# Optimization experiments

Hardware: AMD Instinct MI355X
Metric: run time of the kernel (lower is better)

Reference implementation:

```python
import jax, jax.numpy as jnp
import numpy as np

IN_F = 4096
OUT_F = 4096
BLOCK = 8
N_CENTROIDS = 2048
N_BLOCKS = IN_F // BLOCK  # 512
N_TOKENS = 1024


def setup_inputs() -> dict:
    key = jax.random.key(0)
    k1, k2, k3, k4 = jax.random.split(key, 4)
    x = jax.random.normal(k1, (N_TOKENS, IN_F), dtype=jnp.float32)
    centroids = jax.random.normal(k2, (N_CENTROIDS, BLOCK), dtype=jnp.float32)
    # assignments: block-major layout, length n_blocks * out_features
    assignments = jax.random.randint(k3, (N_BLOCKS * OUT_F,), 0, N_CENTROIDS, dtype=jnp.int32)
    bias = jax.random.normal(k4, (OUT_F,), dtype=jnp.float32) * 0.01
    # counts = bincount(assignments), used only in backward (grad averaging)
    counts = jax.ops.segment_sum(
        jnp.ones_like(assignments, dtype=jnp.float32), assignments,
        num_segments=N_CENTROIDS)
    return {"x": x, "centroids": centroids, "bias": bias,
            "assignments": assignments, "counts": counts}


def reference(x, centroids, bias, assignments, counts):
    # weight = centroids[assignments].reshape(n_blocks, out_f, block)
    #                        .permute(1,0,2).reshape(out_f, in_f)
    w = centroids[assignments]  # [n_blocks*out_f, block]
    w = w.reshape(N_BLOCKS, OUT_F, BLOCK).transpose(1, 0, 2).reshape(OUT_F, IN_F)
    # F.linear(x, weight, bias) = x @ w.T + bias
    return x @ w.T + bias
```

## Files before the change

### kernel.cpp

```cpp
#include <hip/hip_runtime.h>
#include <hip/hip_bf16.h>

#define IN_F   4096
#define OUT_F  4096
#define QBLK   8
#define NBLKS  512
#define NTOK   1024
#define NCENT  2048

#define SPLITK 4
#define KCHUNK (IN_F / SPLITK)
#define KITERS (KCHUNK / 32)

typedef unsigned int u32;
typedef unsigned short u16;
typedef __attribute__((ext_vector_type(8))) short short8;
typedef __attribute__((ext_vector_type(4))) float floatx4;

__device__ __forceinline__ u16 f2bf(float f) {
  union { float f; u32 u; } v; v.f = f;
  u32 u = v.u;
  return (u16)((u + 0x7fffu + ((u >> 16) & 1u)) >> 16);
}

__device__ __forceinline__ void load_lds_16(const void* g, void* l) {
  __builtin_amdgcn_global_load_lds(
      (const __attribute__((address_space(1))) u32*)g,
      (__attribute__((address_space(3))) u32*)l, 16, 0, 0);
}

__global__ __launch_bounds__(256) void cast_bf16_kernel(
    const float* __restrict__ src, u16* __restrict__ dst) {
  int g = blockIdx.x * 256 + threadIdx.x;
  const float4* sv = (const float4*)src;
  float4 a = sv[(size_t)g * 2];
  float4 b = sv[(size_t)g * 2 + 1];
  union { u16 s[8]; uint4 v; } o;
  o.s[0] = f2bf(a.x); o.s[1] = f2bf(a.y); o.s[2] = f2bf(a.z); o.s[3] = f2bf(a.w);
  o.s[4] = f2bf(b.x); o.s[5] = f2bf(b.y); o.s[6] = f2bf(b.z); o.s[7] = f2bf(b.w);
  ((uint4*)dst)[g] = o.v;
}

__global__ __launch_bounds__(256) void cast_swz_kernel(
    const float* __restrict__ src, u16* __restrict__ dst) {
  __shared__ __align__(16) u16 ls[256 * 8];
  const int b = blockIdx.x;
  const int mg = b >> 5;
  const int kq = b & 31;
  const int t = threadIdx.x;
  const int ml = t >> 4;
  const int kbl = t & 15;

  const float* p = src + (size_t)(mg * 16 + ml) * IN_F + kq * 128 + kbl * 8;
  float4 a = ((const float4*)p)[0];
  float4 c = ((const float4*)p)[1];
  union { u16 s[8]; uint4 v; } o;
  o.s[0] = f2bf(a.x); o.s[1] = f2bf(a.y); o.s[2] = f2bf(a.z); o.s[3] = f2bf(a.w);
  o.s[4] = f2bf(c.x); o.s[5] = f2bf(c.y); o.s[6] = f2bf(c.z); o.s[7] = f2bf(c.w);

  const int cidx = (kbl << 4) | (ml ^ kbl);
  *(uint4*)&ls[cidx * 8] = o.v;
  __syncthreads();

  const int g = (t & 0xF0) | ((t & 15) ^ ((t >> 4) & 15));
  uint4* dbase = (uint4*)(dst + (size_t)(mg * 512 + kq * 16) * 128);
  dbase[g] = ((const uint4*)ls)[t];
}

__global__ __launch_bounds__(512, 4) void gemm_fused_kernel(
    const u16* __restrict__ xs,
    const u16* __restrict__ centb,
    const int* __restrict__ assign,
    const float* __restrict__ bias,
    float* __restrict__ out) {
  __shared__ __align__(16) u16 cs[NCENT * 8];
  __shared__ __align__(16) float Cs[128 * 68];

  const int id = blockIdx.x;
  const int m0 = (id & 7) * 128;
  const int n0 = (id >> 3) * 64;

  const int t = threadIdx.x;
  const int lane = t & 63;
  const int wv = t >> 6;
  const int s = wv >> 1;
  const int wm = wv & 1;
  const int quad = lane >> 4;
  const int r16 = lane & 15;
  const int kb0 = s * (KCHUNK >> 3);

#pragma unroll
  for (int it = 0; it < 4; ++it) {
    int c = it * 512 + t;
    load_lds_16(centb + (size_t)c * 8, cs + (size_t)c * 8);
  }

  floatx4 acc[4][4];
#pragma unroll
  for (int i = 0; i < 4; ++i)
#pragma unroll
    for (int j = 0; j < 4; ++j)
#pragma unroll
      for (int r = 0; r < 4; ++r) acc[i][j][r] = 0.0f;

  const int ncol = n0 + r16;

  const char* xA = (const char*)xs +
      ((size_t)((m0 >> 4) + wm * 4) * 512 + kb0) * 256;
  const u32 va = (u32)(quad * 256 + r16 * 16);
  const int* ai = assign + (size_t)kb0 * OUT_F;
  const u32 vi = (u32)(quad * OUT_F + ncol);

  short8 afc[4];
  int idxc[4];
#pragma unroll
  for (int i = 0; i < 4; ++i)
    afc[i] = *(const short8*)(xA + (va + (u32)i * 131072u));
#pragma unroll
  for (int j = 0; j < 4; ++j) idxc[j] = ai[vi + (u32)(j * 16)];

  __syncthreads();

  const short8* csv = (const short8*)cs;
#pragma unroll 2
  for (int kt = 0; kt < KITERS; ++kt) {
    short8 afn[4];
    int idxn[4];
    if (kt + 1 < KITERS) {
      const char* xk = xA + (va + (u32)((kt + 1) * 1024));
#pragma unroll
      for (int i = 0; i < 4; ++i)
        afn[i] = *(const short8*)(xk + (u32)i * 131072u);
      const int* an = ai + (size_t)(kt + 1) * 4 * OUT_F;
#pragma unroll
      for (int j = 0; j < 4; ++j) idxn[j] = an[vi + (u32)(j * 16)];
    }

    short8 bfr[4];
#pragma unroll
    for (int j = 0; j < 4; ++j) bfr[j] = csv[idxc[j]];

#pragma unroll
    for (int i = 0; i < 4; ++i)
#pragma unroll
      for (int j = 0; j < 4; ++j)
        acc[i][j] = __builtin_amdgcn_mfma_f32_16x16x32_bf16(afc[i], bfr[j], acc[i][j], 0, 0, 0);

#pragma unroll
    for (int i = 0; i < 4; ++i) afc[i] = afn[i];
#pragma unroll
    for (int j = 0; j < 4; ++j) idxc[j] = idxn[j];
  }

  const int rbase = wm * 64 + quad * 4;
  if (s == 0) {
#pragma unroll
    for (int i = 0; i < 4; ++i)
#pragma unroll
      for (int j = 0; j < 4; ++j)
#pragma unroll
        for (int r = 0; r < 4; ++r)
          Cs[(rbase + i * 16 + r) * 68 + r16 + j * 16] = acc[i][j][r];
  }
  __syncthreads();
#pragma unroll
  for (int g = 1; g < 4; ++g) {
    if (s == g) {
#pragma unroll
      for (int i = 0; i < 4; ++i)
#pragma unroll
        for (int j = 0; j < 4; ++j)
#pragma unroll
          for (int r = 0; r < 4; ++r)
            Cs[(rbase + i * 16 + r) * 68 + r16 + j * 16] += acc[i][j][r];
    }
    __syncthreads();
  }

  const int c4 = t & 15;
  const float4 b4 = ((const float4*)bias)[(n0 >> 2) + c4];
#pragma unroll
  for (int p = 0; p < 4; ++p) {
    const int rr = p * 32 + (t >> 4);
    float4 v = *(const float4*)&Cs[rr * 68 + c4 * 4];
    v.x += b4.x; v.y += b4.y; v.z += b4.z; v.w += b4.w;
    ((float4*)out)[(((size_t)(m0 + rr) * OUT_F + n0) >> 2) + c4] = v;
  }
}

extern "C" void kernel_launch(void* const* d_in, const int* in_sizes, int n_in,
                              void* d_out, int out_size, void* d_ws, size_t ws_size,
                              hipStream_t stream) {
  const float* x      = (const float*)d_in[0];
  const float* cent   = (const float*)d_in[1];
  const float* bias   = (const float*)d_in[2];
  const int*   assign = (const int*)d_in[3];
  float* out = (float*)d_out;

  const size_t xb_bytes = (size_t)NTOK * IN_F * sizeof(u16);
  u16* xs    = (u16*)d_ws;
  u16* centb = (u16*)((char*)d_ws + xb_bytes);

  hipLaunchKernelGGL(cast_swz_kernel, dim3(64 * 32), dim3(256), 0, stream, x, xs);
  hipLaunchKernelGGL(cast_bf16_kernel, dim3((NCENT * 8 / 8) / 256), dim3(256), 0, stream,
                     cent, centb);
  hipLaunchKernelGGL(gemm_fused_kernel, dim3(512), dim3(512), 0, stream,
                     xs, centb, assign, bias, out);
}
```

Measured before the change: 116.9 us.

## Narrow assignment indices to 16-bit and remap tile order for locality

Adds a pre-pass that converts int32 centroid assignments to uint16 in the workspace, so the GEMM reads half as many bytes of index data per iteration. The block-to-tile mapping also changes so that block ids which are adjacent modulo 8 fall into separate quadrants of M and N, which is meant to improve L2/XCD locality of the shared x and assignment tiles. The cost is an extra kernel launch plus one full read and write of the 8 MB assignment array on every call.

```diff
diff --git a/kernel.cpp b/kernel.cpp
--- a/kernel.cpp
+++ b/kernel.cpp
@@ -41,6 +41,17 @@
   ((uint4*)dst)[g] = o.v;
 }
 
+__global__ __launch_bounds__(256) void cast_idx_kernel(
+    const int* __restrict__ src, u16* __restrict__ dst) {
+  int g = blockIdx.x * 256 + threadIdx.x;
+  int4 a = ((const int4*)src)[(size_t)g * 2];
+  int4 b = ((const int4*)src)[(size_t)g * 2 + 1];
+  union { u16 s[8]; uint4 v; } o;
+  o.s[0] = (u16)a.x; o.s[1] = (u16)a.y; o.s[2] = (u16)a.z; o.s[3] = (u16)a.w;
+  o.s[4] = (u16)b.x; o.s[5] = (u16)b.y; o.s[6] = (u16)b.z; o.s[7] = (u16)b.w;
+  ((uint4*)dst)[g] = o.v;
+}
+
 __global__ __launch_bounds__(256) void cast_swz_kernel(
     const float* __restrict__ src, u16* __restrict__ dst) {
   __shared__ __align__(16) u16 ls[256 * 8];
@@ -70,15 +81,17 @@
 __global__ __launch_bounds__(512, 4) void gemm_fused_kernel(
     const u16* __restrict__ xs,
     const u16* __restrict__ centb,
-    const int* __restrict__ assign,
+    const u16* __restrict__ assign,
     const float* __restrict__ bias,
     float* __restrict__ out) {
   __shared__ __align__(16) u16 cs[NCENT * 8];
   __shared__ __align__(16) float Cs[128 * 68];
 
   const int id = blockIdx.x;
-  const int m0 = (id & 7) * 128;
-  const int n0 = (id >> 3) * 64;
+  const int c = id & 7;
+  const int sub = id >> 3;
+  const int m0 = (c >> 1) * 256 + (sub & 1) * 128;
+  const int n0 = (c & 1) * 2048 + (sub >> 1) * 64;
 
   const int t = threadIdx.x;
   const int lane = t & 63;
@@ -91,8 +104,8 @@
 
 #pragma unroll
   for (int it = 0; it < 4; ++it) {
-    int c = it * 512 + t;
-    load_lds_16(centb + (size_t)c * 8, cs + (size_t)c * 8);
+    int cc = it * 512 + t;
+    load_lds_16(centb + (size_t)cc * 8, cs + (size_t)cc * 8);
   }
 
   floatx4 acc[4][4];
@@ -108,7 +121,7 @@
   const char* xA = (const char*)xs +
       ((size_t)((m0 >> 4) + wm * 4) * 512 + kb0) * 256;
   const u32 va = (u32)(quad * 256 + r16 * 16);
-  const int* ai = assign + (size_t)kb0 * OUT_F;
+  const u16* ai = assign + (size_t)kb0 * OUT_F;
   const u32 vi = (u32)(quad * OUT_F + ncol);
 
   short8 afc[4];
@@ -117,7 +130,7 @@
   for (int i = 0; i < 4; ++i)
     afc[i] = *(const short8*)(xA + (va + (u32)i * 131072u));
 #pragma unroll
-  for (int j = 0; j < 4; ++j) idxc[j] = ai[vi + (u32)(j * 16)];
+  for (int j = 0; j < 4; ++j) idxc[j] = (int)ai[vi + (u32)(j * 16)];
 
   __syncthreads();
 
@@ -131,9 +144,9 @@
 #pragma unroll
       for (int i = 0; i < 4; ++i)
         afn[i] = *(const short8*)(xk + (u32)i * 131072u);
-      const int* an = ai + (size_t)(kt + 1) * 4 * OUT_F;
-#pragma unroll
-      for (int j = 0; j < 4; ++j) idxn[j] = an[vi + (u32)(j * 16)];
+      const u16* an = ai + (size_t)(kt + 1) * 4 * OUT_F;
+#pragma unroll
+      for (int j = 0; j < 4; ++j) idxn[j] = (int)an[vi + (u32)(j * 16)];
     }
 
     short8 bfr[4];
@@ -197,13 +210,17 @@
   const int*   assign = (const int*)d_in[3];
   float* out = (float*)d_out;
 
-  const size_t xb_bytes = (size_t)NTOK * IN_F * sizeof(u16);
-  u16* xs    = (u16*)d_ws;
-  u16* centb = (u16*)((char*)d_ws + xb_bytes);
+  const size_t xb_bytes   = (size_t)NTOK * IN_F * sizeof(u16);
+  const size_t cent_bytes = (size_t)NCENT * 8 * sizeof(u16);
+  u16* xs       = (u16*)d_ws;
+  u16* centb    = (u16*)((char*)d_ws + xb_bytes);
+  u16* assign16 = (u16*)((char*)d_ws + xb_bytes + cent_bytes);
 
   hipLaunchKernelGGL(cast_swz_kernel, dim3(64 * 32), dim3(256), 0, stream, x, xs);
   hipLaunchKernelGGL(cast_bf16_kernel, dim3((NCENT * 8 / 8) / 256), dim3(256), 0, stream,
                      cent, centb);
+  hipLaunchKernelGGL(cast_idx_kernel, dim3((NBLKS * OUT_F / 8) / 256), dim3(256), 0, stream,
+                     assign, assign16);
   hipLaunchKernelGGL(gemm_fused_kernel, dim3(512), dim3(512), 0, stream,
-                     xs, centb, assign, bias, out);
-}
+                     xs, centb, assign16, bias, out);
+}
```

New measurement: 119.7 us. 1.02x slower.
